# Kernel optimization log

Hardware: AMD Instinct MI355X
Metric: run time of the kernel (lower is better)

## Reference

```python
import jax, jax.numpy as jnp
import numpy as np

N_NODES = 100000
N_EDGES = 1600000
IN_CH = 128
HID = 128
OUT_CH = 64
N_GRAPHS = 512


def gcn_conv(x, edge_index, W, b):
    # GCNConv (PyG defaults): add self-loops, symmetric normalization
    # out = D^{-1/2} (A + I) D^{-1/2} X W + b
    n = x.shape[0]
    loop = jnp.arange(n, dtype=edge_index.dtype)
    src = jnp.concatenate([edge_index[0], loop])
    dst = jnp.concatenate([edge_index[1], loop])
    deg = jax.ops.segment_sum(jnp.ones_like(dst, x.dtype), dst, num_segments=n)
    dinv = jnp.where(deg > 0, jax.lax.rsqrt(deg), jnp.zeros_like(deg))
    norm = dinv[src] * dinv[dst]            # [E+N]
    h = x @ W                                # [N, out] transform first (dense GEMM)
    msg = h[src] * norm[:, None]             # gather + scale  [E+N, out]
    return jax.ops.segment_sum(msg, dst, num_segments=n) + b


def global_mean_pool(x, batch, num_graphs):
    sums = jax.ops.segment_sum(x, batch, num_segments=num_graphs)
    cnts = jax.ops.segment_sum(jnp.ones_like(batch, x.dtype), batch, num_segments=num_graphs)
    return sums / jnp.maximum(cnts, 1.0)[:, None]


def setup_inputs() -> dict:
    key = jax.random.key(0)
    ks = jax.random.split(key, 12)
    x = jax.random.normal(ks[0], (N_NODES, IN_CH), dtype=jnp.float32)
    edge_index = jax.random.randint(ks[1], (2, N_EDGES), 0, N_NODES, dtype=jnp.int64)
    batch = jnp.sort(jax.random.randint(ks[2], (N_NODES,), 0, N_GRAPHS, dtype=jnp.int64))
    def glorot(k, fi, fo):
        s = float(np.sqrt(6.0 / (fi + fo)))
        return jax.random.uniform(k, (fi, fo), jnp.float32, -s, s)
    W1 = glorot(ks[3], IN_CH, HID); b1 = jnp.zeros((HID,), jnp.float32)
    W2 = glorot(ks[4], HID, HID);   b2 = jnp.zeros((HID,), jnp.float32)
    W3 = glorot(ks[5], HID, HID);   b3 = jnp.zeros((HID,), jnp.float32)
    W4 = glorot(ks[6], HID, OUT_CH); b4 = jnp.zeros((OUT_CH,), jnp.float32)
    return {"x": x, "edge_index": edge_index, "batch": batch,
            "W1": W1, "b1": b1, "W2": W2, "b2": b2,
            "W3": W3, "b3": b3, "W4": W4, "b4": b4}


def reference(x, edge_index, batch, W1, b1, W2, b2, W3, b3, W4, b4):
    h = jax.nn.relu(gcn_conv(x, edge_index, W1, b1))
    h = jax.nn.relu(gcn_conv(h, edge_index, W2, b2))
    g = global_mean_pool(h, batch, N_GRAPHS)           # [G, HID]
    # MLP head; Dropout(0.2) is identity in eval mode
    g = jax.nn.relu(g @ W3 + b3)
    return g @ W4 + b4                                  # [G, OUT_CH]
```

## Files before the change

kernel.cpp:

```cpp
#include <hip/hip_runtime.h>

#define NN 100000
#define EE 1600000
#define CH 128
#define NG 512
#define OC 64

#define CSH 10
#define NCB 98
#define PBLK 256
#define PCHUNK 6250
#define SCAP 128

#define O_DINV   0
#define O_ROWS   100032
#define O_CNT    200064
#define O_PART   225152
#define O_OFFS   225280
#define O_START  225408
#define O_CSR    225984
#define O_HS     2726016
#define O_STG    9126080
#define O_WT1    9126080
#define O_WT2    9142464
#define O_A1     14800448

typedef __attribute__((ext_vector_type(8))) short short8v;
typedef __attribute__((ext_vector_type(4))) float float4v;

static __device__ __forceinline__ unsigned short f2bf(float x) {
  unsigned u = __float_as_uint(x);
  return (unsigned short)((u + 0x7FFFu + ((u >> 16) & 1u)) >> 16);
}
static __device__ __forceinline__ float bf2f(unsigned short h) {
  return __uint_as_float((unsigned)h << 16);
}
static __device__ __forceinline__ unsigned pack2(float a, float b) {
  return (unsigned)f2bf(a) | ((unsigned)f2bf(b) << 16);
}
static __device__ __forceinline__ float bflo(unsigned v) {
  return __uint_as_float(v << 16);
}
static __device__ __forceinline__ float bfhi(unsigned v) {
  return __uint_as_float(v & 0xFFFF0000u);
}

__global__ __launch_bounds__(1024) void k_part(const int* __restrict__ src,
                                               const int* __restrict__ dst,
                                               int* __restrict__ cnt,
                                               unsigned* __restrict__ stg) {
  __shared__ int hist[NCB];
  __shared__ int lcur[NCB];
  __shared__ unsigned lout[PCHUNK];
  int t = threadIdx.x;
  int e0 = blockIdx.x * PCHUNK;
  if (t < NCB) { hist[t] = 0; lcur[t] = 0; }
  __syncthreads();
  for (int e = e0 + t; e < e0 + PCHUNK; e += 1024)
    atomicAdd(&hist[dst[e] >> CSH], 1);
  __syncthreads();
  if (t == 0) {
    int s = 0;
    for (int i = 0; i < NCB; ++i) { int v = hist[i]; hist[i] = s; s += v; }
  }
  __syncthreads();
  for (int e = e0 + t; e < e0 + PCHUNK; e += 1024) {
    int d = dst[e];
    int b = d >> CSH;
    int p = hist[b] + atomicAdd(&lcur[b], 1);
    lout[p] = (unsigned)src[e] | ((unsigned)(d & 1023) << 17);
  }
  __syncthreads();
  int w = t >> 6, lane = t & 63;
  unsigned* mystg = stg + (size_t)blockIdx.x * NCB * SCAP;
  for (int b = w; b < NCB; b += 16) {
    int beg = hist[b];
    int end = (b == NCB - 1) ? PCHUNK : hist[b + 1];
    int n = min(end - beg, SCAP);
    for (int i = lane; i < n; i += 64) mystg[b * SCAP + i] = lout[beg + i];
    if (lane == 0) cnt[blockIdx.x * NCB + b] = n;
  }
}

__global__ __launch_bounds__(1024) void k_count(const unsigned* __restrict__ stg,
                                                const int* __restrict__ cnt,
                                                int* __restrict__ rows,
                                                int* __restrict__ part,
                                                float* __restrict__ dinv) {
  __shared__ int ldeg[1024];
  __shared__ int s[1024];
  int b = blockIdx.x;
  int t = threadIdx.x;
  int w = t >> 6, lane = t & 63;
  int gid = (b << CSH) + t;
  ldeg[t] = 0;
  __syncthreads();
  for (int blk = w; blk < PBLK; blk += 16) {
    int c = cnt[blk * NCB + b];
    const unsigned* p = stg + ((size_t)blk * NCB + b) * SCAP;
    for (int e = lane; e < c; e += 64) atomicAdd(&ldeg[p[e] >> 17], 1);
  }
  __syncthreads();
  int v = ldeg[t];
  if (gid < NN) dinv[gid] = rsqrtf((float)(v + 1));
  int pdeg = (v + 7) & ~7;
  s[t] = pdeg;
  __syncthreads();
  for (int off = 1; off < 1024; off <<= 1) {
    int u = (t >= off) ? s[t - off] : 0;
    __syncthreads();
    if (t >= off) s[t] += u;
    __syncthreads();
  }
  if (gid < NN) rows[gid] = s[t] - pdeg;
  if (t == 1023) part[b] = s[t];
}

__global__ void k_scan_part(const int* __restrict__ part, int* __restrict__ offs) {
  __shared__ int s[128];
  int t = threadIdx.x;
  int v = (t < NCB) ? part[t] : 0;
  s[t] = v;
  __syncthreads();
  for (int off = 1; off < 128; off <<= 1) {
    int u = (t >= off) ? s[t - off] : 0;
    __syncthreads();
    if (t >= off) s[t] += u;
    __syncthreads();
  }
  if (t < NCB) offs[t] = s[t] - v;
}

__global__ void k_scan_add(int* __restrict__ rows, const int* __restrict__ offs,
                           const int* __restrict__ part,
                           const int* __restrict__ batch, int* __restrict__ start) {
  int i = blockIdx.x * 256 + threadIdx.x;
  if (i >= NN) return;
  rows[i] += offs[i >> 10];
  if (i == 0) rows[NN] = offs[NCB - 1] + part[NCB - 1];
  int b = batch[i];
  int prev = (i == 0) ? -1 : batch[i - 1];
  for (int g = prev + 1; g <= b; ++g) start[g] = i;
  if (i == NN - 1)
    for (int g = b + 1; g <= NG; ++g) start[g] = NN;
}

__global__ __launch_bounds__(1024) void k_place(const unsigned* __restrict__ stg,
                                                const int* __restrict__ cnt,
                                                const int* __restrict__ rows,
                                                int* __restrict__ csr) {
  __shared__ int lrow[1024];
  __shared__ int lcur[1024];
  int b = blockIdx.x;
  int t = threadIdx.x;
  int w = t >> 6, lane = t & 63;
  int gid = (b << CSH) + t;
  lrow[t] = (gid < NN) ? rows[gid] : 0;
  lcur[t] = 0;
  __syncthreads();
  for (int blk = w; blk < PBLK; blk += 16) {
    int c = cnt[blk * NCB + b];
    const unsigned* p = stg + ((size_t)blk * NCB + b) * SCAP;
    for (int e = lane; e < c; e += 64) {
      unsigned x = p[e];
      int ld = x >> 17;
      int q = atomicAdd(&lcur[ld], 1);
      csr[lrow[ld] + q] = (int)(x & 0x1FFFFu);
    }
  }
  __syncthreads();
  int d = lcur[t];
  int pd = (d + 7) & ~7;
  int base = lrow[t];
  for (int i = d; i < pd; ++i) csr[base + i] = NN;
}

__global__ void k_wsplit(const float* __restrict__ W1, const float* __restrict__ W2,
                         unsigned short* __restrict__ wt1,
                         unsigned short* __restrict__ wt2) {
  int id = blockIdx.x * 256 + threadIdx.x;
  const float* W = (id < 16384) ? W1 : W2;
  unsigned short* wt = (id < 16384) ? wt1 : wt2;
  int i = id & 16383;
  int k = i >> 7, n = i & 127;
  float w = W[i];
  unsigned short h = f2bf(w);
  unsigned short l = f2bf(w - bf2f(h));
  wt[n * 128 + k] = h;
  wt[16384 + n * 128 + k] = l;
}

__global__ __launch_bounds__(256) void k_gemm_mfma(
    const float* __restrict__ X, const unsigned short* __restrict__ wth,
    const unsigned short* __restrict__ wtl, const float* __restrict__ dinv,
    unsigned short* __restrict__ Hs) {
  __shared__ __align__(16) unsigned short sWh[64 * 136];
  __shared__ __align__(16) unsigned short sWl[64 * 136];
  __shared__ __align__(16) unsigned short sXh[128 * 40];
  __shared__ __align__(16) unsigned short sXl[128 * 40];

  const int t = threadIdx.x;
  const int w = t >> 6, lane = t & 63;
  const int quad = lane >> 4, lr = lane & 15;
  const int row0 = blockIdx.x * 128;
  const int col0 = blockIdx.y * 64;

  if (blockIdx.x == 0 && blockIdx.y == 0 && t < 64)
    *(unsigned*)&Hs[(size_t)NN * CH + t * 2] = 0u;

#pragma unroll
  for (int j = 0; j < 8; ++j) {
    int id = t + j * 256;
    int n = id >> 5, kk = (id & 31) * 4;
    *(ushort4*)&sWh[n * 136 + kk] = *(const ushort4*)&wth[(col0 + n) * 128 + kk];
    *(ushort4*)&sWl[n * 136 + kk] = *(const ushort4*)&wtl[(col0 + n) * 128 + kk];
  }

  float4v acc[2][4];
#pragma unroll
  for (int mi = 0; mi < 2; ++mi)
#pragma unroll
    for (int ni = 0; ni < 4; ++ni) acc[mi][ni] = (float4v){0.f, 0.f, 0.f, 0.f};

  for (int ks = 0; ks < 4; ++ks) {
    const int k0 = ks * 32;
    if (ks) __syncthreads();
#pragma unroll
    for (int i = 0; i < 4; ++i) {
      int row = i * 32 + (t >> 3);
      int seg = t & 7;
      int gr = row0 + row;
      float4 xv = {0.f, 0.f, 0.f, 0.f};
      if (gr < NN) xv = *(const float4*)&X[(size_t)gr * CH + k0 + seg * 4];
      ushort4 h, l;
      h.x = f2bf(xv.x); l.x = f2bf(xv.x - bf2f(h.x));
      h.y = f2bf(xv.y); l.y = f2bf(xv.y - bf2f(h.y));
      h.z = f2bf(xv.z); l.z = f2bf(xv.z - bf2f(h.z));
      h.w = f2bf(xv.w); l.w = f2bf(xv.w - bf2f(h.w));
      *(ushort4*)&sXh[row * 40 + seg * 4] = h;
      *(ushort4*)&sXl[row * 40 + seg * 4] = l;
    }
    __syncthreads();

    short8v ah[2], al[2];
#pragma unroll
    for (int mi = 0; mi < 2; ++mi) {
      int r = w * 32 + mi * 16 + lr;
      ah[mi] = *(const short8v*)&sXh[r * 40 + quad * 8];
      al[mi] = *(const short8v*)&sXl[r * 40 + quad * 8];
    }
#pragma unroll
    for (int ni = 0; ni < 4; ++ni) {
      int n = ni * 16 + lr;
      short8v bh = *(const short8v*)&sWh[n * 136 + k0 + quad * 8];
      short8v bl = *(const short8v*)&sWl[n * 136 + k0 + quad * 8];
#pragma unroll
      for (int mi = 0; mi < 2; ++mi) {
        acc[mi][ni] = __builtin_amdgcn_mfma_f32_16x16x32_bf16(ah[mi], bh, acc[mi][ni], 0, 0, 0);
        acc[mi][ni] = __builtin_amdgcn_mfma_f32_16x16x32_bf16(ah[mi], bl, acc[mi][ni], 0, 0, 0);
        acc[mi][ni] = __builtin_amdgcn_mfma_f32_16x16x32_bf16(al[mi], bh, acc[mi][ni], 0, 0, 0);
      }
    }
  }

#pragma unroll
  for (int mi = 0; mi < 2; ++mi) {
#pragma unroll
    for (int r = 0; r < 4; ++r) {
      int grow = row0 + w * 32 + mi * 16 + quad * 4 + r;
      if (grow < NN) {
        float d = dinv[grow];
#pragma unroll
        for (int ni = 0; ni < 4; ++ni)
          Hs[(size_t)grow * CH + col0 + ni * 16 + lr] = f2bf(d * acc[mi][ni][r]);
      }
    }
  }
}

__global__ __launch_bounds__(256) void k_gemm_bf(
    const unsigned short* __restrict__ A, const unsigned short* __restrict__ wth,
    const unsigned short* __restrict__ wtl, const float* __restrict__ dinv,
    unsigned short* __restrict__ Hs) {
  __shared__ __align__(16) unsigned short sWh[64 * 136];
  __shared__ __align__(16) unsigned short sWl[64 * 136];
  __shared__ __align__(16) unsigned short sA[128 * 40];

  const int t = threadIdx.x;
  const int w = t >> 6, lane = t & 63;
  const int quad = lane >> 4, lr = lane & 15;
  const int row0 = blockIdx.x * 128;
  const int col0 = blockIdx.y * 64;

  if (blockIdx.x == 0 && blockIdx.y == 0 && t < 64)
    *(unsigned*)&Hs[(size_t)NN * CH + t * 2] = 0u;

#pragma unroll
  for (int j = 0; j < 8; ++j) {
    int id = t + j * 256;
    int n = id >> 5, kk = (id & 31) * 4;
    *(ushort4*)&sWh[n * 136 + kk] = *(const ushort4*)&wth[(col0 + n) * 128 + kk];
    *(ushort4*)&sWl[n * 136 + kk] = *(const ushort4*)&wtl[(col0 + n) * 128 + kk];
  }

  float4v acc[2][4];
#pragma unroll
  for (int mi = 0; mi < 2; ++mi)
#pragma unroll
    for (int ni = 0; ni < 4; ++ni) acc[mi][ni] = (float4v){0.f, 0.f, 0.f, 0.f};

  for (int ks = 0; ks < 4; ++ks) {
    const int k0 = ks * 32;
    if (ks) __syncthreads();
#pragma unroll
    for (int i = 0; i < 2; ++i) {
      int id = t + i * 256;
      int row = id >> 2, seg = id & 3;
      int gr = row0 + row;
      ushort4 v = {0, 0, 0, 0};
      if (gr < NN) v = *(const ushort4*)&A[(size_t)gr * CH + k0 + seg * 8];
      *(ushort4*)&sA[row * 40 + seg * 8] = v;
      ushort4 v2 = {0, 0, 0, 0};
      if (gr < NN) v2 = *(const ushort4*)&A[(size_t)gr * CH + k0 + seg * 8 + 4];
      *(ushort4*)&sA[row * 40 + seg * 8 + 4] = v2;
    }
    __syncthreads();

    short8v ah[2];
#pragma unroll
    for (int mi = 0; mi < 2; ++mi) {
      int r = w * 32 + mi * 16 + lr;
      ah[mi] = *(const short8v*)&sA[r * 40 + quad * 8];
    }
#pragma unroll
    for (int ni = 0; ni < 4; ++ni) {
      int n = ni * 16 + lr;
      short8v bh = *(const short8v*)&sWh[n * 136 + k0 + quad * 8];
      short8v bl = *(const short8v*)&sWl[n * 136 + k0 + quad * 8];
#pragma unroll
      for (int mi = 0; mi < 2; ++mi) {
        acc[mi][ni] = __builtin_amdgcn_mfma_f32_16x16x32_bf16(ah[mi], bh, acc[mi][ni], 0, 0, 0);
        acc[mi][ni] = __builtin_amdgcn_mfma_f32_16x16x32_bf16(ah[mi], bl, acc[mi][ni], 0, 0, 0);
      }
    }
  }

#pragma unroll
  for (int mi = 0; mi < 2; ++mi) {
#pragma unroll
    for (int r = 0; r < 4; ++r) {
      int grow = row0 + w * 32 + mi * 16 + quad * 4 + r;
      if (grow < NN) {
        float d = dinv[grow];
#pragma unroll
        for (int ni = 0; ni < 4; ++ni)
          Hs[(size_t)grow * CH + col0 + ni * 16 + lr] = f2bf(d * acc[mi][ni][r]);
      }
    }
  }
}

__global__ __launch_bounds__(256) void k_aggregate(
    const unsigned* __restrict__ H, const int* __restrict__ rows,
    const int* __restrict__ csr, const float* __restrict__ dinv,
    const float* __restrict__ bias, unsigned* __restrict__ out) {
  int node = blockIdx.x * 4 + (threadIdx.x >> 6);
  int lane = threadIdx.x & 63;
  if (node >= NN) return;
  float bx = bias[2 * lane], by = bias[2 * lane + 1];
  unsigned sv = H[((unsigned)node << 6) | lane];
  float ax = bflo(sv), ay = bfhi(sv);
  int e0 = rows[node], e1 = rows[node + 1];
  if (e1 > e0) {
    unsigned va[8], vb[8];
#pragma unroll
    for (int k = 0; k < 8; ++k)
      va[k] = H[((unsigned)csr[e0 + k] << 6) | lane];
    for (int base = e0 + 8; base < e1; base += 8) {
#pragma unroll
      for (int k = 0; k < 8; ++k)
        vb[k] = H[((unsigned)csr[base + k] << 6) | lane];
#pragma unroll
      for (int k = 0; k < 8; ++k) { ax += bflo(va[k]); ay += bfhi(va[k]); }
#pragma unroll
      for (int k = 0; k < 8; ++k) va[k] = vb[k];
    }
#pragma unroll
    for (int k = 0; k < 8; ++k) { ax += bflo(va[k]); ay += bfhi(va[k]); }
  }
  float d = dinv[node];
  float ox = fmaxf(fmaf(d, ax, bx), 0.f);
  float oy = fmaxf(fmaf(d, ay, by), 0.f);
  out[((unsigned)node << 6) | lane] = pack2(ox, oy);
}

__global__ __launch_bounds__(256) void k_head(
    const unsigned short* __restrict__ A, const int* __restrict__ start,
    const float* __restrict__ W3, const float* __restrict__ b3,
    const float* __restrict__ W4, const float* __restrict__ b4,
    float* __restrict__ out) {
  __shared__ float pooled[128];
  __shared__ float part[128];
  __shared__ float g1[128];
  int g = blockIdx.x;
  int c = threadIdx.x & 127;
  int half = threadIdx.x >> 7;
  int s0 = start[g], s1 = start[g + 1];
  float sum = 0.f;
  for (int i = s0 + half; i < s1; i += 2)
    sum += bf2f(A[(size_t)i * CH + c]);
  if (half) part[c] = sum;
  __syncthreads();
  if (!half) {
    float n = fmaxf((float)(s1 - s0), 1.0f);
    pooled[c] = (sum + part[c]) / n;
  }
  __syncthreads();
  if (threadIdx.x < 128) {
    float acc = b3[c];
    for (int k = 0; k < 128; ++k) acc += pooled[k] * W3[k * CH + c];
    g1[c] = fmaxf(acc, 0.f);
  }
  __syncthreads();
  if (threadIdx.x < 64) {
    float acc = b4[threadIdx.x];
    for (int k = 0; k < 128; ++k) acc += g1[k] * W4[k * OC + threadIdx.x];
    out[(size_t)g * OC + threadIdx.x] = acc;
  }
}

extern "C" void kernel_launch(void* const* d_in, const int* in_sizes, int n_in,
                              void* d_out, int out_size, void* d_ws, size_t ws_size,
                              hipStream_t stream) {
  const float* X   = (const float*)d_in[0];
  const int* ei    = (const int*)d_in[1];
  const int* batch = (const int*)d_in[2];
  const float* W1  = (const float*)d_in[3];
  const float* b1  = (const float*)d_in[4];
  const float* W2  = (const float*)d_in[5];
  const float* b2  = (const float*)d_in[6];
  const float* W3  = (const float*)d_in[7];
  const float* b3  = (const float*)d_in[8];
  const float* W4  = (const float*)d_in[9];
  const float* b4  = (const float*)d_in[10];
  float* out = (float*)d_out;
  float* ws = (float*)d_ws;

  const int* src = ei;
  const int* dst = ei + EE;

  float* dinv = ws + O_DINV;
  int* rows   = (int*)(ws + O_ROWS);
  int* cnt    = (int*)(ws + O_CNT);
  int* part   = (int*)(ws + O_PART);
  int* offs   = (int*)(ws + O_OFFS);
  int* start  = (int*)(ws + O_START);
  int* csr    = (int*)(ws + O_CSR);
  unsigned short* Hs = (unsigned short*)(ws + O_HS);
  unsigned* stg = (unsigned*)(ws + O_STG);
  unsigned short* wt1 = (unsigned short*)(ws + O_WT1);
  unsigned short* wt2 = (unsigned short*)(ws + O_WT2);
  unsigned short* A1 = (unsigned short*)(ws + O_A1);

  k_part<<<PBLK, 1024, 0, stream>>>(src, dst, cnt, stg);
  k_count<<<NCB, 1024, 0, stream>>>(stg, cnt, rows, part, dinv);
  k_scan_part<<<1, 128, 0, stream>>>(part, offs);
  k_scan_add<<<(NN + 255) / 256, 256, 0, stream>>>(rows, offs, part, batch, start);
  k_place<<<NCB, 1024, 0, stream>>>(stg, cnt, rows, csr);
  k_wsplit<<<128, 256, 0, stream>>>(W1, W2, wt1, wt2);

  dim3 ggrid((NN + 127) / 128, 2);
  k_gemm_mfma<<<ggrid, 256, 0, stream>>>(X, wt1, wt1 + 16384, dinv, Hs);
  k_aggregate<<<(NN + 3) / 4, 256, 0, stream>>>((const unsigned*)Hs, rows, csr, dinv, b1, (unsigned*)A1);
  k_gemm_bf<<<ggrid, 256, 0, stream>>>(A1, wt2, wt2 + 16384, dinv, Hs);
  k_aggregate<<<(NN + 3) / 4, 256, 0, stream>>>((const unsigned*)Hs, rows, csr, dinv, b2, (unsigned*)A1);

  k_head<<<NG, 256, 0, stream>>>(A1, start, W3, b3, W4, b4, out);
}
```

Before: 376.4 us.

## Split aggregation channels across XCD groups with edge-parallel sub-wavefronts

Aggregation now gives each wavefront a 16-channel slice (64 bytes) of one node instead of all 128 channels. The four 16-lane subgroups each take a different edge and are reduced with shuffles. Block indices are remapped so that each pair of XCDs handles one channel quarter. The aim is to shrink each XCD's working set of H so it fits better in that XCD's L2 and to raise gather parallelism. The cost is four times as many blocks and two shuffle reductions. It also relies on edge counts being padded to multiples of 8, as the original code already assumed.

```diff
diff --git a/kernel.cpp b/kernel.cpp
--- a/kernel.cpp
+++ b/kernel.cpp
@@ -361,37 +361,66 @@
 }
 
 __global__ __launch_bounds__(256) void k_aggregate(
-    const unsigned* __restrict__ H, const int* __restrict__ rows,
+    const unsigned* __restrict__ H1, const int* __restrict__ rows,
     const int* __restrict__ csr, const float* __restrict__ dinv,
     const float* __restrict__ bias, unsigned* __restrict__ out) {
-  int node = blockIdx.x * 4 + (threadIdx.x >> 6);
+  unsigned b = blockIdx.x;
+  unsigned xcd = b & 7u;
+  unsigned g = xcd >> 1;
+  unsigned nb = (b >> 3) * 2 + (xcd & 1);
+  int node = (int)(nb * 4) + (threadIdx.x >> 6);
+  if (node >= NN) return;
   int lane = threadIdx.x & 63;
-  if (node >= NN) return;
-  float bx = bias[2 * lane], by = bias[2 * lane + 1];
-  unsigned sv = H[((unsigned)node << 6) | lane];
-  float ax = bflo(sv), ay = bfhi(sv);
+  int sub = lane >> 4;
+  unsigned li = (unsigned)(lane & 15);
+  unsigned chbase = g * 16 + li;
+  const unsigned* Hb = H1 + chbase;
+  float a0 = 0.f, a1 = 0.f;
   int e0 = rows[node], e1 = rows[node + 1];
-  if (e1 > e0) {
-    unsigned va[8], vb[8];
-#pragma unroll
-    for (int k = 0; k < 8; ++k)
-      va[k] = H[((unsigned)csr[e0 + k] << 6) | lane];
-    for (int base = e0 + 8; base < e1; base += 8) {
-#pragma unroll
-      for (int k = 0; k < 8; ++k)
-        vb[k] = H[((unsigned)csr[base + k] << 6) | lane];
-#pragma unroll
-      for (int k = 0; k < 8; ++k) { ax += bflo(va[k]); ay += bfhi(va[k]); }
-#pragma unroll
-      for (int k = 0; k < 8; ++k) va[k] = vb[k];
-    }
-#pragma unroll
-    for (int k = 0; k < 8; ++k) { ax += bflo(va[k]); ay += bfhi(va[k]); }
-  }
+  int nr = (e1 - e0) >> 3;
+  if (nr) {
+    const int* cp = csr + e0 + sub;
+    unsigned va0, va1, vb0, vb1;
+
+#define LOADQ(p0, p1)                                                       \
+  do {                                                                      \
+    unsigned s0_ = (unsigned)cp[0], s1_ = (unsigned)cp[4];                  \
+    p0 = Hb[s0_ << 6];                                                      \
+    p1 = Hb[s1_ << 6];                                                      \
+    cp += 8;                                                                \
+  } while (0)
+
+#define ACCQ(p0, p1)                                                        \
+  do {                                                                      \
+    a0 += bflo(p0); a1 += bfhi(p0);                                         \
+    a0 += bflo(p1); a1 += bfhi(p1);                                         \
+  } while (0)
+
+    LOADQ(va0, va1);
+    int rem = nr - 1;
+    while (rem >= 2) {
+      LOADQ(vb0, vb1); ACCQ(va0, va1);
+      LOADQ(va0, va1); ACCQ(vb0, vb1);
+      rem -= 2;
+    }
+    if (rem) { LOADQ(vb0, vb1); ACCQ(va0, va1); ACCQ(vb0, vb1); }
+    else     { ACCQ(va0, va1); }
+#undef LOADQ
+#undef ACCQ
+  }
+  a0 += __shfl_xor(a0, 16);
+  a1 += __shfl_xor(a1, 16);
+  a0 += __shfl_xor(a0, 32);
+  a1 += __shfl_xor(a1, 32);
+  unsigned sv = Hb[(unsigned)node << 6];
+  a0 += bflo(sv);
+  a1 += bfhi(sv);
   float d = dinv[node];
-  float ox = fmaxf(fmaf(d, ax, bx), 0.f);
-  float oy = fmaxf(fmaf(d, ay, by), 0.f);
-  out[((unsigned)node << 6) | lane] = pack2(ox, oy);
+  float2 bv = *(const float2*)&bias[chbase << 1];
+  float o0 = fmaxf(fmaf(d, a0, bv.x), 0.f);
+  float o1 = fmaxf(fmaf(d, a1, bv.y), 0.f);
+  if (sub == 0)
+    out[((unsigned)node << 6) | chbase] = pack2(o0, o1);
 }
 
 __global__ __launch_bounds__(256) void k_head(
@@ -471,9 +500,9 @@
 
   dim3 ggrid((NN + 127) / 128, 2);
   k_gemm_mfma<<<ggrid, 256, 0, stream>>>(X, wt1, wt1 + 16384, dinv, Hs);
-  k_aggregate<<<(NN + 3) / 4, 256, 0, stream>>>((const unsigned*)Hs, rows, csr, dinv, b1, (unsigned*)A1);
+  k_aggregate<<<100000, 256, 0, stream>>>((const unsigned*)Hs, rows, csr, dinv, b1, (unsigned*)A1);
   k_gemm_bf<<<ggrid, 256, 0, stream>>>(A1, wt2, wt2 + 16384, dinv, Hs);
-  k_aggregate<<<(NN + 3) / 4, 256, 0, stream>>>((const unsigned*)Hs, rows, csr, dinv, b2, (unsigned*)A1);
+  k_aggregate<<<100000, 256, 0, stream>>>((const unsigned*)Hs, rows, csr, dinv, b2, (unsigned*)A1);
 
   k_head<<<NG, 256, 0, stream>>>(A1, start, W3, b3, W4, b4, out);
 }
```

After: 511.8 us. 1.36x slower.

## Slice feature matrices into 16-channel column planes and aggregate per slice

Applied to the files above, without the earlier changes.

Stores the hidden feature matrices as eight column slices of 16 bf16 channels, each laid out node-major, so a gathered neighbour row fits a 32-byte segment. The aggregation kernel now assigns each block to one slice and 32 nodes. Within a wavefront, 8 edge groups of 8 lanes gather in parallel and are combined by shuffle reduction. The GEMM writers, the GEMM A loader and the pooling head are adapted to the new layout. The aim is better cache-line locality for the random gathers, at the cost of more blocks, gathering the CSR edge lists once per slice, and idle lanes on output writes.

```diff
diff --git a/kernel.cpp b/kernel.cpp
--- a/kernel.cpp
+++ b/kernel.cpp
@@ -24,6 +24,11 @@
 #define O_WT1    9126080
 #define O_WT2    9142464
 #define O_A1     14800448
+
+#define HSL_US 1600016u
+#define HSL_U32 800008u
+#define ASL_US 1600000u
+#define ASL_U32 800000u
 
 typedef __attribute__((ext_vector_type(8))) short short8v;
 typedef __attribute__((ext_vector_type(4))) float float4v;
@@ -205,8 +210,10 @@
   const int row0 = blockIdx.x * 128;
   const int col0 = blockIdx.y * 64;
 
-  if (blockIdx.x == 0 && blockIdx.y == 0 && t < 64)
-    *(unsigned*)&Hs[(size_t)NN * CH + t * 2] = 0u;
+  if (blockIdx.x == 0 && blockIdx.y == 0 && t < 64) {
+    unsigned* Hu = (unsigned*)Hs;
+    Hu[(size_t)(t >> 3) * HSL_U32 + (unsigned)NN * 8u + (t & 7)] = 0u;
+  }
 
 #pragma unroll
   for (int j = 0; j < 8; ++j) {
@@ -272,7 +279,8 @@
         float d = dinv[grow];
 #pragma unroll
         for (int ni = 0; ni < 4; ++ni)
-          Hs[(size_t)grow * CH + col0 + ni * 16 + lr] = f2bf(d * acc[mi][ni][r]);
+          Hs[(size_t)(col0 / 16 + ni) * HSL_US + (size_t)grow * 16 + lr] =
+              f2bf(d * acc[mi][ni][r]);
       }
     }
   }
@@ -292,8 +300,10 @@
   const int row0 = blockIdx.x * 128;
   const int col0 = blockIdx.y * 64;
 
-  if (blockIdx.x == 0 && blockIdx.y == 0 && t < 64)
-    *(unsigned*)&Hs[(size_t)NN * CH + t * 2] = 0u;
+  if (blockIdx.x == 0 && blockIdx.y == 0 && t < 64) {
+    unsigned* Hu = (unsigned*)Hs;
+    Hu[(size_t)(t >> 3) * HSL_U32 + (unsigned)NN * 8u + (t & 7)] = 0u;
+  }
 
 #pragma unroll
   for (int j = 0; j < 8; ++j) {
@@ -312,17 +322,18 @@
   for (int ks = 0; ks < 4; ++ks) {
     const int k0 = ks * 32;
     if (ks) __syncthreads();
-#pragma unroll
-    for (int i = 0; i < 2; ++i) {
-      int id = t + i * 256;
-      int row = id >> 2, seg = id & 3;
+    {
+      int row = t >> 1, half = t & 1;
       int gr = row0 + row;
-      ushort4 v = {0, 0, 0, 0};
-      if (gr < NN) v = *(const ushort4*)&A[(size_t)gr * CH + k0 + seg * 8];
-      *(ushort4*)&sA[row * 40 + seg * 8] = v;
-      ushort4 v2 = {0, 0, 0, 0};
-      if (gr < NN) v2 = *(const ushort4*)&A[(size_t)gr * CH + k0 + seg * 8 + 4];
-      *(ushort4*)&sA[row * 40 + seg * 8 + 4] = v2;
+      uint4 v0 = {0u, 0u, 0u, 0u}, v1 = {0u, 0u, 0u, 0u};
+      if (gr < NN) {
+        const unsigned short* src =
+            A + (size_t)(2 * ks + half) * ASL_US + (size_t)gr * 16;
+        v0 = *(const uint4*)src;
+        v1 = *(const uint4*)(src + 8);
+      }
+      *(uint4*)&sA[row * 40 + half * 16] = v0;
+      *(uint4*)&sA[row * 40 + half * 16 + 8] = v1;
     }
     __syncthreads();
 
@@ -354,7 +365,8 @@
         float d = dinv[grow];
 #pragma unroll
         for (int ni = 0; ni < 4; ++ni)
-          Hs[(size_t)grow * CH + col0 + ni * 16 + lr] = f2bf(d * acc[mi][ni][r]);
+          Hs[(size_t)(col0 / 16 + ni) * HSL_US + (size_t)grow * 16 + lr] =
+              f2bf(d * acc[mi][ni][r]);
       }
     }
   }
@@ -364,34 +376,44 @@
     const unsigned* __restrict__ H, const int* __restrict__ rows,
     const int* __restrict__ csr, const float* __restrict__ dinv,
     const float* __restrict__ bias, unsigned* __restrict__ out) {
-  int node = blockIdx.x * 4 + (threadIdx.x >> 6);
+  unsigned b = blockIdx.x;
+  unsigned s = b & 7u;
+  unsigned nb = b >> 3;
   int lane = threadIdx.x & 63;
-  if (node >= NN) return;
-  float bx = bias[2 * lane], by = bias[2 * lane + 1];
-  unsigned sv = H[((unsigned)node << 6) | lane];
-  float ax = bflo(sv), ay = bfhi(sv);
-  int e0 = rows[node], e1 = rows[node + 1];
-  if (e1 > e0) {
-    unsigned va[8], vb[8];
-#pragma unroll
-    for (int k = 0; k < 8; ++k)
-      va[k] = H[((unsigned)csr[e0 + k] << 6) | lane];
-    for (int base = e0 + 8; base < e1; base += 8) {
-#pragma unroll
-      for (int k = 0; k < 8; ++k)
-        vb[k] = H[((unsigned)csr[base + k] << 6) | lane];
-#pragma unroll
-      for (int k = 0; k < 8; ++k) { ax += bflo(va[k]); ay += bfhi(va[k]); }
-#pragma unroll
-      for (int k = 0; k < 8; ++k) va[k] = vb[k];
-    }
-#pragma unroll
-    for (int k = 0; k < 8; ++k) { ax += bflo(va[k]); ay += bfhi(va[k]); }
-  }
-  float d = dinv[node];
-  float ox = fmaxf(fmaf(d, ax, bx), 0.f);
-  float oy = fmaxf(fmaf(d, ay, by), 0.f);
-  out[((unsigned)node << 6) | lane] = pack2(ox, oy);
+  int ss = lane >> 3;
+  unsigned ln = (unsigned)(lane & 7);
+  const unsigned* Hb = H + (size_t)s * HSL_U32 + ln;
+  unsigned obase = s * ASL_U32 + ln;
+  float2 bv = *(const float2*)&bias[(s * 8u + ln) * 2];
+  int node0 = (int)(nb * 32) + (threadIdx.x >> 6) * 8;
+  for (int node = node0; node < node0 + 8; ++node) {
+    float a0 = 0.f, a1 = 0.f;
+    int e0 = rows[node], e1 = rows[node + 1];
+    if (e1 > e0) {
+      const int* cp = csr + e0 + ss;
+      unsigned srcv = (unsigned)cp[0];
+      cp += 8;
+      for (int e = e0 + 8; e < e1; e += 8) {
+        unsigned nsrc = (unsigned)cp[0];
+        cp += 8;
+        unsigned sv = Hb[srcv << 3];
+        a0 += bflo(sv); a1 += bfhi(sv);
+        srcv = nsrc;
+      }
+      unsigned sv = Hb[srcv << 3];
+      a0 += bflo(sv); a1 += bfhi(sv);
+    }
+    a0 += __shfl_xor(a0, 8);  a1 += __shfl_xor(a1, 8);
+    a0 += __shfl_xor(a0, 16); a1 += __shfl_xor(a1, 16);
+    a0 += __shfl_xor(a0, 32); a1 += __shfl_xor(a1, 32);
+    unsigned sv = Hb[(unsigned)node << 3];
+    a0 += bflo(sv); a1 += bfhi(sv);
+    float d = dinv[node];
+    float o0 = fmaxf(fmaf(d, a0, bv.x), 0.f);
+    float o1 = fmaxf(fmaf(d, a1, bv.y), 0.f);
+    if (lane < 8)
+      out[obase + ((unsigned)node << 3)] = pack2(o0, o1);
+  }
 }
 
 __global__ __launch_bounds__(256) void k_head(
@@ -406,9 +428,10 @@
   int c = threadIdx.x & 127;
   int half = threadIdx.x >> 7;
   int s0 = start[g], s1 = start[g + 1];
+  const unsigned short* Ac = A + (size_t)(c >> 4) * ASL_US + (c & 15);
   float sum = 0.f;
   for (int i = s0 + half; i < s1; i += 2)
-    sum += bf2f(A[(size_t)i * CH + c]);
+    sum += bf2f(Ac[(size_t)i * 16]);
   if (half) part[c] = sum;
   __syncthreads();
   if (!half) {
@@ -471,9 +494,9 @@
 
   dim3 ggrid((NN + 127) / 128, 2);
   k_gemm_mfma<<<ggrid, 256, 0, stream>>>(X, wt1, wt1 + 16384, dinv, Hs);
-  k_aggregate<<<(NN + 3) / 4, 256, 0, stream>>>((const unsigned*)Hs, rows, csr, dinv, b1, (unsigned*)A1);
+  k_aggregate<<<25000, 256, 0, stream>>>((const unsigned*)Hs, rows, csr, dinv, b1, (unsigned*)A1);
   k_gemm_bf<<<ggrid, 256, 0, stream>>>(A1, wt2, wt2 + 16384, dinv, Hs);
-  k_aggregate<<<(NN + 3) / 4, 256, 0, stream>>>((const unsigned*)Hs, rows, csr, dinv, b2, (unsigned*)A1);
+  k_aggregate<<<25000, 256, 0, stream>>>((const unsigned*)Hs, rows, csr, dinv, b2, (unsigned*)A1);
 
   k_head<<<NG, 256, 0, stream>>>(A1, start, W3, b3, W4, b4, out);
 }
```

Result: slower. 584.5 us (+55.3%).
